# Optimization experiments

Measured on AMD Instinct MI355X. Metric: run time of the kernel, lower is better.

Reference implementation:

```python
import jax, jax.numpy as jnp
import numpy as np

CHEB_K = 3  # from init_kwargs

def _layernorm(v, g, b, eps=1e-12):
    mu = jnp.mean(v, axis=-1, keepdims=True)
    var = jnp.var(v, axis=-1, keepdims=True)  # biased, matches torch LayerNorm
    return (v - mu) * jax.lax.rsqrt(var + eps) * g + b

def setup_inputs() -> dict:
    key = jax.random.key(0)
    ks = jax.random.split(key, 5)
    B, N, D_IN, D_OUT, E = 64, 2048, 64, 64, 16
    return {
        "x": jax.random.normal(ks[0], (B, N, D_IN), dtype=jnp.float32),
        "node_embeddings": jax.random.normal(ks[1], (N, E), dtype=jnp.float32),
        "time_embeddings": jax.random.normal(ks[2], (E,), dtype=jnp.float32),
        "weights_pool": jax.random.normal(ks[3], (E, CHEB_K, D_IN, D_OUT), dtype=jnp.float32) * 0.1,
        "bias_pool": jax.random.normal(ks[4], (E, D_OUT), dtype=jnp.float32) * 0.1,
        "ln_gamma": jnp.ones((E,), dtype=jnp.float32),
        "ln_beta": jnp.zeros((E,), dtype=jnp.float32),
    }

def reference(x, node_embeddings, time_embeddings, weights_pool, bias_pool, ln_gamma, ln_beta):
    N = node_embeddings.shape[0]
    # dropout in eval mode -> identity
    ne = _layernorm(node_embeddings + time_embeddings[None, :], ln_gamma, ln_beta)  # [N,E]
    supports0 = jax.nn.softmax(ne @ ne.T, axis=1)  # [N,N]
    support_set = [jnp.eye(N, dtype=x.dtype), supports0]
    for _ in range(2, CHEB_K):
        support_set.append(2.0 * supports0 @ support_set[-1] - support_set[-2])
    supports = jnp.stack(support_set, axis=0)  # [K,N,N]
    weights = jnp.einsum('nd,dkio->nkio', ne, weights_pool)  # [N,K,I,O]
    bias = ne @ bias_pool  # [N,O]
    x_g = jnp.einsum('knm,bmc->bnkc', supports, x)  # [B,N,K,I]
    return jnp.einsum('bnki,nkio->bno', x_g, weights) + bias  # [B,N,O]
```

## Files before the change

### kernel.cpp

```cpp
#include <hip/hip_runtime.h>
#include <stdint.h>

typedef unsigned short u16;
typedef __attribute__((ext_vector_type(8))) short   bf16x8;
typedef __attribute__((ext_vector_type(4))) float   f32x4;
typedef __attribute__((ext_vector_type(4))) u16     u16x4;
typedef __attribute__((ext_vector_type(8))) u16     u16x8;

#define NN 2048
#define BB 64
#define DD 64
#define XSTRIDE (NN*DD)

__device__ __forceinline__ float bf2f(u16 u) {
    union { unsigned int i; float f; } v; v.i = ((unsigned int)u) << 16; return v.f;
}
__device__ __forceinline__ u16 f2bf(float f) {
    union { float f; unsigned int i; } v; v.f = f;
    unsigned int u = v.i;
    return (u16)((u + 0x7fffu + ((u >> 16) & 1u)) >> 16);
}

typedef __attribute__((address_space(3))) unsigned int lds_u32_t;
typedef const __attribute__((address_space(1))) unsigned int g_u32_t;
__device__ __forceinline__ void gload_lds16(const void* g, void* l) {
    __builtin_amdgcn_global_load_lds((g_u32_t*)(uintptr_t)g, (lds_u32_t*)(uintptr_t)l, 16, 0, 0);
}

__global__ __launch_bounds__(256) void k_ln(const float* __restrict__ nodee,
                                            const float* __restrict__ timee,
                                            const float* __restrict__ gamma,
                                            const float* __restrict__ beta,
                                            float* __restrict__ ne,
                                            u16* __restrict__ neb) {
    int n = blockIdx.x * 256 + threadIdx.x;
    float v[16]; float mu = 0.f;
    const float4* p = (const float4*)(nodee + (long)n * 16);
#pragma unroll
    for (int i = 0; i < 4; i++) {
        float4 q = p[i];
        v[i*4+0]=q.x; v[i*4+1]=q.y; v[i*4+2]=q.z; v[i*4+3]=q.w;
    }
#pragma unroll
    for (int e = 0; e < 16; e++) { v[e] += timee[e]; mu += v[e]; }
    mu *= (1.f/16.f);
    float var = 0.f;
#pragma unroll
    for (int e = 0; e < 16; e++) { float d = v[e]-mu; var += d*d; }
    var *= (1.f/16.f);
    float rs = rsqrtf(var + 1e-12f);
    float4* o = (float4*)(ne + (long)n * 16);
    u16x8 nb[2];
#pragma unroll
    for (int i = 0; i < 4; i++) {
        float4 q;
        q.x = (v[i*4+0]-mu)*rs*gamma[i*4+0] + beta[i*4+0];
        q.y = (v[i*4+1]-mu)*rs*gamma[i*4+1] + beta[i*4+1];
        q.z = (v[i*4+2]-mu)*rs*gamma[i*4+2] + beta[i*4+2];
        q.w = (v[i*4+3]-mu)*rs*gamma[i*4+3] + beta[i*4+3];
        o[i] = q;
        nb[i>>1][(i&1)*4+0] = f2bf(q.x); nb[i>>1][(i&1)*4+1] = f2bf(q.y);
        nb[i>>1][(i&1)*4+2] = f2bf(q.z); nb[i>>1][(i&1)*4+3] = f2bf(q.w);
    }
    u16x8 z;
#pragma unroll
    for (int j = 0; j < 8; j++) z[j] = 0;
    u16x8* ob = (u16x8*)&neb[(long)n * 32];
    ob[0] = nb[0]; ob[1] = nb[1]; ob[2] = z; ob[3] = z;
}

__global__ __launch_bounds__(256) void k_wperm(const float* __restrict__ wp,
                                               u16* __restrict__ wpP) {
    int j = blockIdx.x * 256 + threadIdx.x;
    int o = j / 192, ki = j - o * 192;
    int src = ki * 64 + o;
    u16x8 ov[4];
#pragma unroll
    for (int e = 0; e < 16; e++) ov[e>>3][e&7] = f2bf(wp[(long)e*12288 + src]);
#pragma unroll
    for (int e = 0; e < 8; e++) { ov[2][e] = 0; ov[3][e] = 0; }
    u16x8* dst = (u16x8*)&wpP[(long)j * 32];
    dst[0]=ov[0]; dst[1]=ov[1]; dst[2]=ov[2]; dst[3]=ov[3];
}

__global__ __launch_bounds__(256) void k_softmax(const float* __restrict__ ne,
                                                 u16* __restrict__ S) {
    __shared__ float row[2048];
    __shared__ float red[8];
    int n = blockIdx.x, t = threadIdx.x;
    int wave = t >> 6, lane = t & 63;
    f32x4 nev[4];
#pragma unroll
    for (int i = 0; i < 4; i++) nev[i] = *(const f32x4*)&ne[n*16 + i*4];
    float lmax = -1e30f;
    for (int m = t; m < 2048; m += 256) {
        const f32x4* p = (const f32x4*)&ne[m*16];
        f32x4 d4 = nev[0]*p[0] + nev[1]*p[1] + nev[2]*p[2] + nev[3]*p[3];
        float d = d4[0]+d4[1]+d4[2]+d4[3];
        row[m] = d;
        lmax = fmaxf(lmax, d);
    }
#pragma unroll
    for (int off = 32; off > 0; off >>= 1) lmax = fmaxf(lmax, __shfl_xor(lmax, off));
    if (lane == 0) red[wave] = lmax;
    __syncthreads();
    float gmax = fmaxf(fmaxf(red[0], red[1]), fmaxf(red[2], red[3]));
    float lsum = 0.f;
    for (int m = t; m < 2048; m += 256) {
        float ev = __expf(row[m] - gmax);
        row[m] = ev;
        lsum += ev;
    }
#pragma unroll
    for (int off = 32; off > 0; off >>= 1) lsum += __shfl_xor(lsum, off);
    __syncthreads();
    if (lane == 0) red[wave] = lsum;
    __syncthreads();
    float inv = 1.f / (red[0]+red[1]+red[2]+red[3]);
    for (int m = t; m < 2048; m += 256)
        S[(long)n*2048 + m] = f2bf(row[m] * inv);
}

__global__ __launch_bounds__(256) void k_permute(const float* __restrict__ x,
                                                 u16* __restrict__ Xpt) {
    __shared__ u16 T[64][72];
    int bid = blockIdx.x;
    int b = bid >> 5, m0 = (bid & 31) * 64;
    int t = threadIdx.x;
#pragma unroll
    for (int it = 0; it < 4; it++) {
        int fi = it*256 + t;
        int row = fi >> 4, c4 = (fi & 15) * 4;
        float4 v = *(const float4*)&x[(long)b*XSTRIDE + (m0+row)*64 + c4];
        T[c4+0][row] = f2bf(v.x); T[c4+1][row] = f2bf(v.y);
        T[c4+2][row] = f2bf(v.z); T[c4+3][row] = f2bf(v.w);
    }
    __syncthreads();
#pragma unroll
    for (int it = 0; it < 2; it++) {
        int ch = it*256 + t;
        int c = ch >> 3, m8 = (ch & 7) * 8;
        u16x8 v = *(const u16x8*)&T[c][m8];
        *(u16x8*)&Xpt[(long)(b*64 + c)*2048 + m0 + m8] = v;
    }
}

__global__ __launch_bounds__(256) void k_gemm_bt(const u16* __restrict__ A,
                                                 const u16* __restrict__ Bt,
                                                 u16* __restrict__ C,
                                                 int M, int Ncols, int K) {
    __shared__ __align__(16) u16 As[128*32];
    __shared__ __align__(16) u16 Bs[128*32];
    const int t = threadIdx.x;
    const int wave = t >> 6, lane = t & 63;
    const int l15 = lane & 15, lhi = lane >> 4;
    const int m0 = blockIdx.y * 128;
    const int n0 = blockIdx.x * 128;
    const int wr = wave >> 1, wc = wave & 1;
    f32x4 acc[4][4] = {};
    const int srow = t >> 2;
    const int sk = (t & 3) * 8;
    const u16* gA = A + (long)(m0 + srow) * K + sk;
    const u16* gB = Bt + (long)(n0 + srow) * K + sk;
    const long half = (long)64 * K;
    u16* lA = As + wave * 512;
    u16* lB = Bs + wave * 512;
    const int aoff = (wr*64 + l15)*32 + lhi*8;
    const int boff = (wc*64 + l15)*32 + lhi*8;
    for (int k0 = 0; k0 < K; k0 += 32) {
        gload_lds16(gA + k0,        lA);
        gload_lds16(gA + k0 + half, lA + 2048);
        gload_lds16(gB + k0,        lB);
        gload_lds16(gB + k0 + half, lB + 2048);
        __syncthreads();
        bf16x8 af[4], bv[4];
#pragma unroll
        for (int m = 0; m < 4; m++) af[m] = *(const bf16x8*)&As[aoff + m*512];
#pragma unroll
        for (int q = 0; q < 4; q++) bv[q] = *(const bf16x8*)&Bs[boff + q*512];
#pragma unroll
        for (int m = 0; m < 4; m++)
#pragma unroll
            for (int q = 0; q < 4; q++)
                acc[m][q] = __builtin_amdgcn_mfma_f32_16x16x32_bf16(af[m], bv[q], acc[m][q], 0, 0, 0);
        __syncthreads();
    }
#pragma unroll
    for (int m = 0; m < 4; m++) {
        int row = m0 + wr*64 + m*16 + lhi*4;
#pragma unroll
        for (int q = 0; q < 4; q++) {
            int col = n0 + wc*64 + q*16 + l15;
#pragma unroll
            for (int r = 0; r < 4; r++)
                C[(long)(row + r) * Ncols + col] = f2bf(acc[m][q][r]);
        }
    }
}

__global__ __launch_bounds__(512, 1) void k_gemm_big(const u16* __restrict__ A,
                                                     const u16* __restrict__ Bt,
                                                     u16* __restrict__ C,
                                                     u16* __restrict__ Ct,
                                                     int M, int Ncols, int K) {
    __shared__ __align__(16) u16 LB[73728];
    const int t = threadIdx.x;
    const int wave = t >> 6, lane = t & 63;
    const int l15 = lane & 15, lhi = lane >> 4;
    const int nwg = gridDim.x * gridDim.y;
    const int wgid = blockIdx.y * gridDim.x + blockIdx.x;
    const int swz = (wgid & 7) * (nwg >> 3) + (wgid >> 3);
    const int by = swz / gridDim.x, bx = swz - by * gridDim.x;
    const int m0 = by * 128, n0 = bx * 256;
    const int wr = wave >> 2, wc = wave & 3;
    const int NT = K >> 6;
    f32x4 acc[4][4] = {};

    const int srow = t >> 3;
    const int sswz = ((t & 7) ^ (srow & 7)) * 8;
    const u16* gA0 = A  + (long)(m0 + srow) * K + sswz;
    const u16* gB0 = Bt + (long)(n0 + srow) * K + sswz;
    const long rP = (long)64 * K;
    const int ldsW = wave * 512;

    int curA = 0,     nxtA = 8192,  tgtA = 16384;
    int curB = 24576, nxtB = 40960, tgtB = 57344;

    gload_lds16(gA0,           &LB[curA + 0*4096 + ldsW]);
    gload_lds16(gA0 + rP,      &LB[curA + 1*4096 + ldsW]);
#pragma unroll
    for (int r = 0; r < 4; r++) gload_lds16(gB0 + r*rP,      &LB[curB + r*4096 + ldsW]);
    gload_lds16(gA0 + 64,      &LB[nxtA + 0*4096 + ldsW]);
    gload_lds16(gA0 + rP + 64, &LB[nxtA + 1*4096 + ldsW]);
#pragma unroll
    for (int r = 0; r < 4; r++) gload_lds16(gB0 + r*rP + 64, &LB[nxtB + r*4096 + ldsW]);
    asm volatile("s_waitcnt vmcnt(6)" ::: "memory");
    __builtin_amdgcn_s_barrier();
    asm volatile("" ::: "memory");

    const int rsw = l15 & 7;
    const int sw0 = (lhi ^ rsw) * 8;
    const int sw1 = ((4 + lhi) ^ rsw) * 8;
    const int abase = (wr*64 + l15) * 64;
    const int bbase = (wc*64 + l15) * 64;

#pragma unroll 1
    for (int tt = 0; tt < NT; tt++) {
        const bool stg = (tt + 2 < NT);
        const long ko2 = (long)((tt + 2) << 6);
        {
            bf16x8 af[4], bv[4];
#pragma unroll
            for (int m = 0; m < 4; m++) af[m] = *(const bf16x8*)&LB[curA + abase + m*1024 + sw0];
#pragma unroll
            for (int q = 0; q < 4; q++) bv[q] = *(const bf16x8*)&LB[curB + bbase + q*1024 + sw0];
            if (stg) {
                gload_lds16(gA0 + ko2,      &LB[tgtA + 0*4096 + ldsW]);
                gload_lds16(gA0 + rP + ko2, &LB[tgtA + 1*4096 + ldsW]);
                gload_lds16(gB0 + ko2,      &LB[tgtB + 0*4096 + ldsW]);
            }
            __builtin_amdgcn_s_setprio(1);
#pragma unroll
            for (int m = 0; m < 4; m++)
#pragma unroll
                for (int q = 0; q < 4; q++)
                    acc[m][q] = __builtin_amdgcn_mfma_f32_16x16x32_bf16(af[m], bv[q], acc[m][q], 0, 0, 0);
            __builtin_amdgcn_s_setprio(0);
        }
        {
            bf16x8 af[4], bv[4];
#pragma unroll
            for (int m = 0; m < 4; m++) af[m] = *(const bf16x8*)&LB[curA + abase + m*1024 + sw1];
#pragma unroll
            for (int q = 0; q < 4; q++) bv[q] = *(const bf16x8*)&LB[curB + bbase + q*1024 + sw1];
            if (stg) {
                gload_lds16(gB0 + 1*rP + ko2, &LB[tgtB + 1*4096 + ldsW]);
                gload_lds16(gB0 + 2*rP + ko2, &LB[tgtB + 2*4096 + ldsW]);
                gload_lds16(gB0 + 3*rP + ko2, &LB[tgtB + 3*4096 + ldsW]);
            }
            __builtin_amdgcn_s_setprio(1);
#pragma unroll
            for (int m = 0; m < 4; m++)
#pragma unroll
                for (int q = 0; q < 4; q++)
                    acc[m][q] = __builtin_amdgcn_mfma_f32_16x16x32_bf16(af[m], bv[q], acc[m][q], 0, 0, 0);
            __builtin_amdgcn_s_setprio(0);
        }
        asm volatile("" ::: "memory");
        if (stg)                asm volatile("s_waitcnt vmcnt(6)" ::: "memory");
        else if (tt + 1 < NT)   asm volatile("s_waitcnt vmcnt(0)" ::: "memory");
        if (tt + 1 < NT) {
            __builtin_amdgcn_s_barrier();
            asm volatile("" ::: "memory");
        }
        int ta = curA; curA = nxtA; nxtA = tgtA; tgtA = ta;
        int tb = curB; curB = nxtB; nxtB = tgtB; tgtB = tb;
    }
#pragma unroll
    for (int m = 0; m < 4; m++) {
        int row = m0 + wr*64 + m*16 + lhi*4;
#pragma unroll
        for (int q = 0; q < 4; q++) {
            int col = n0 + wc*64 + q*16 + l15;
#pragma unroll
            for (int r = 0; r < 4; r++)
                C[(long)(row + r) * Ncols + col] = f2bf(acc[m][q][r]);
        }
    }
    if (Ct != nullptr) {
        __syncthreads();
#pragma unroll
        for (int m = 0; m < 4; m++) {
            int rowb = wr*64 + m*16 + lhi*4;
#pragma unroll
            for (int q = 0; q < 4; q++) {
                int col = wc*64 + q*16 + l15;
                u16x4 p;
                p[0]=f2bf(acc[m][q][0]); p[1]=f2bf(acc[m][q][1]);
                p[2]=f2bf(acc[m][q][2]); p[3]=f2bf(acc[m][q][3]);
                *(u16x4*)&LB[col*136 + rowb] = p;
            }
        }
        __syncthreads();
        const int j16 = t >> 4, ch = (t & 15) * 8;
#pragma unroll
        for (int p = 0; p < 8; p++) {
            int j = p*32 + j16;
            u16x8 v = *(const u16x8*)&LB[j*136 + ch];
            *(u16x8*)&Ct[(long)(n0 + j)*M + m0 + ch] = v;
        }
    }
}

__global__ __launch_bounds__(256) void k_final(const float* __restrict__ x,
                                               const u16* __restrict__ Y1,
                                               const u16* __restrict__ Y2,
                                               const u16* __restrict__ Wt,
                                               const float* __restrict__ ne,
                                               const float* __restrict__ bp,
                                               float* __restrict__ out) {
    __shared__ __align__(16) u16 Al[64*200];
    __shared__ __align__(16) u16 Wl[64*200];
    __shared__ float biasl[64];
    int n = blockIdx.x;
    int t = threadIdx.x;
    int wave = t >> 6, lane = t & 63;
    int l15 = lane & 15, lhi = lane >> 4;
#pragma unroll
    for (int it = 0; it < 6; it++) {
        int ch = it*256 + t;
        int o = ch / 24, kl = (ch % 24) * 8;
        u16x8 v = *(const u16x8*)&Wt[(long)n*12288 + ch*8];
        *(u16x8*)&Wl[o*200 + kl] = v;
    }
    float xs[16];
#pragma unroll
    for (int it = 0; it < 4; it++) {
        int fi = it*256 + t;
        int b = fi >> 4, i4 = (fi & 15) * 4;
        float4 v = *(const float4*)&x[(long)b*XSTRIDE + n*64 + i4];
        xs[it*4+0]=v.x; xs[it*4+1]=v.y; xs[it*4+2]=v.z; xs[it*4+3]=v.w;
        u16x4 p; p[0]=f2bf(v.x); p[1]=f2bf(v.y); p[2]=f2bf(v.z); p[3]=f2bf(v.w);
        *(u16x4*)&Al[b*200 + i4] = p;
    }
#pragma unroll
    for (int it = 0; it < 2; it++) {
        int ch = it*256 + t;
        int b = ch >> 3, i8 = (ch & 7)*8;
        u16x8 v = *(const u16x8*)&Y1[(long)n*4096 + ch*8];
        *(u16x8*)&Al[b*200 + 64 + i8] = v;
    }
#pragma unroll
    for (int it = 0; it < 4; it++) {
        int fi = it*256 + t;
        int b = fi >> 4, i4 = (fi & 15)*4;
        u16x4 y = *(const u16x4*)&Y2[(long)n*4096 + fi*4];
        u16x4 p;
#pragma unroll
        for (int j = 0; j < 4; j++) p[j] = f2bf(2.f*bf2f(y[j]) - xs[it*4+j]);
        *(u16x4*)&Al[b*200 + 128 + i4] = p;
    }
    if (t < 64) {
        float s = 0.f;
#pragma unroll
        for (int e = 0; e < 16; e++) s += ne[n*16+e] * bp[e*64 + t];
        biasl[t] = s;
    }
    __syncthreads();
    f32x4 acc[4] = {};
#pragma unroll
    for (int kk = 0; kk < 6; kk++) {
        bf16x8 bv = *(const bf16x8*)&Wl[(wave*16 + l15)*200 + kk*32 + lhi*8];
#pragma unroll
        for (int m = 0; m < 4; m++) {
            bf16x8 av = *(const bf16x8*)&Al[(m*16 + l15)*200 + kk*32 + lhi*8];
            acc[m] = __builtin_amdgcn_mfma_f32_16x16x32_bf16(av, bv, acc[m], 0, 0, 0);
        }
    }
    int o = wave*16 + l15;
    float bias = biasl[o];
#pragma unroll
    for (int m = 0; m < 4; m++) {
        int brow = m*16 + lhi*4;
#pragma unroll
        for (int r = 0; r < 4; r++)
            out[(long)(brow + r)*XSTRIDE + n*64 + o] = acc[m][r] + bias;
    }
}

extern "C" void kernel_launch(void* const* d_in, const int* in_sizes, int n_in,
                              void* d_out, int out_size, void* d_ws, size_t ws_size,
                              hipStream_t stream) {
    const float* x     = (const float*)d_in[0];
    const float* nodee = (const float*)d_in[1];
    const float* timee = (const float*)d_in[2];
    const float* wp    = (const float*)d_in[3];
    const float* bp    = (const float*)d_in[4];
    const float* gamma = (const float*)d_in[5];
    const float* beta  = (const float*)d_in[6];
    float* out = (float*)d_out;

    char* ws = (char*)d_ws;
    float* ne  = (float*)(ws);
    u16* S     = (u16*)(ws + 131072);
    u16* Xpt   = (u16*)(ws + 8519680);
    u16* Y1    = (u16*)(ws + 25296896);
    u16* Y1t   = (u16*)(ws + 42074112);
    u16* Y2    = (u16*)(ws + 58851328);
    u16* Wt    = (u16*)(ws + 75628544);
    u16* neb   = (u16*)(ws + 58851328);
    u16* wpP   = (u16*)(ws + 58851328 + 131072);
    if (ws_size < (size_t)125960192) return;

    k_ln      <<<8,    256, 0, stream>>>(nodee, timee, gamma, beta, ne, neb);
    k_wperm   <<<48,   256, 0, stream>>>(wp, wpP);
    k_gemm_bt <<<dim3(96,16), 256, 0, stream>>>(neb, wpP, Wt, 2048, 12288, 32);
    k_softmax <<<2048, 256, 0, stream>>>(ne, S);
    k_permute <<<2048, 256, 0, stream>>>(x, Xpt);
    k_gemm_big<<<dim3(16,16), 512, 0, stream>>>(S, Xpt, Y1, Y1t, 2048, 4096, 2048);
    k_gemm_big<<<dim3(16,16), 512, 0, stream>>>(S, Y1t, Y2, (u16*)nullptr, 2048, 4096, 2048);
    k_final   <<<2048, 256, 0, stream>>>(x, Y1, Y2, Wt, ne, bp, out);
}
```

Before: 150.7 us.

## Split K across wave pairs in big GEMM with LDS reduction

```diff
diff --git a/kernel.cpp b/kernel.cpp
--- a/kernel.cpp
+++ b/kernel.cpp
@@ -198,7 +198,7 @@
     }
 }
 
-__global__ __launch_bounds__(512, 1) void k_gemm_big(const u16* __restrict__ A,
+__global__ __launch_bounds__(512, 2) void k_gemm_big(const u16* __restrict__ A,
                                                      const u16* __restrict__ Bt,
                                                      u16* __restrict__ C,
                                                      u16* __restrict__ Ct,
@@ -212,9 +212,11 @@
     const int swz = (wgid & 7) * (nwg >> 3) + (wgid >> 3);
     const int by = swz / gridDim.x, bx = swz - by * gridDim.x;
     const int m0 = by * 128, n0 = bx * 256;
-    const int wr = wave >> 2, wc = wave & 3;
+    const int kwv = wave & 1;
+    const int ws  = wave >> 1;
+    const int wr = ws >> 1, wc = ws & 1;
     const int NT = K >> 6;
-    f32x4 acc[4][4] = {};
+    f32x4 acc[4][8] = {};
 
     const int srow = t >> 3;
     const int sswz = ((t & 7) ^ (srow & 7)) * 8;
@@ -239,53 +241,34 @@
     asm volatile("" ::: "memory");
 
     const int rsw = l15 & 7;
-    const int sw0 = (lhi ^ rsw) * 8;
-    const int sw1 = ((4 + lhi) ^ rsw) * 8;
-    const int abase = (wr*64 + l15) * 64;
-    const int bbase = (wc*64 + l15) * 64;
+    const int swk = ((kwv*4 + lhi) ^ rsw) * 8;
+    const int abase = (wr*64  + l15) * 64;
+    const int bbase = (wc*128 + l15) * 64;
 
 #pragma unroll 1
     for (int tt = 0; tt < NT; tt++) {
         const bool stg = (tt + 2 < NT);
         const long ko2 = (long)((tt + 2) << 6);
-        {
-            bf16x8 af[4], bv[4];
-#pragma unroll
-            for (int m = 0; m < 4; m++) af[m] = *(const bf16x8*)&LB[curA + abase + m*1024 + sw0];
-#pragma unroll
-            for (int q = 0; q < 4; q++) bv[q] = *(const bf16x8*)&LB[curB + bbase + q*1024 + sw0];
-            if (stg) {
-                gload_lds16(gA0 + ko2,      &LB[tgtA + 0*4096 + ldsW]);
-                gload_lds16(gA0 + rP + ko2, &LB[tgtA + 1*4096 + ldsW]);
-                gload_lds16(gB0 + ko2,      &LB[tgtB + 0*4096 + ldsW]);
-            }
-            __builtin_amdgcn_s_setprio(1);
-#pragma unroll
-            for (int m = 0; m < 4; m++)
-#pragma unroll
-                for (int q = 0; q < 4; q++)
-                    acc[m][q] = __builtin_amdgcn_mfma_f32_16x16x32_bf16(af[m], bv[q], acc[m][q], 0, 0, 0);
-            __builtin_amdgcn_s_setprio(0);
-        }
-        {
-            bf16x8 af[4], bv[4];
-#pragma unroll
-            for (int m = 0; m < 4; m++) af[m] = *(const bf16x8*)&LB[curA + abase + m*1024 + sw1];
-#pragma unroll
-            for (int q = 0; q < 4; q++) bv[q] = *(const bf16x8*)&LB[curB + bbase + q*1024 + sw1];
-            if (stg) {
-                gload_lds16(gB0 + 1*rP + ko2, &LB[tgtB + 1*4096 + ldsW]);
-                gload_lds16(gB0 + 2*rP + ko2, &LB[tgtB + 2*4096 + ldsW]);
-                gload_lds16(gB0 + 3*rP + ko2, &LB[tgtB + 3*4096 + ldsW]);
-            }
-            __builtin_amdgcn_s_setprio(1);
-#pragma unroll
-            for (int m = 0; m < 4; m++)
-#pragma unroll
-                for (int q = 0; q < 4; q++)
-                    acc[m][q] = __builtin_amdgcn_mfma_f32_16x16x32_bf16(af[m], bv[q], acc[m][q], 0, 0, 0);
-            __builtin_amdgcn_s_setprio(0);
-        }
+        bf16x8 af[4], bv[8];
+#pragma unroll
+        for (int m = 0; m < 4; m++) af[m] = *(const bf16x8*)&LB[curA + abase + m*1024 + swk];
+#pragma unroll
+        for (int q = 0; q < 8; q++) bv[q] = *(const bf16x8*)&LB[curB + bbase + q*1024 + swk];
+        if (stg) {
+            gload_lds16(gA0 + ko2,        &LB[tgtA + 0*4096 + ldsW]);
+            gload_lds16(gA0 + rP + ko2,   &LB[tgtA + 1*4096 + ldsW]);
+            gload_lds16(gB0 + ko2,        &LB[tgtB + 0*4096 + ldsW]);
+            gload_lds16(gB0 + 1*rP + ko2, &LB[tgtB + 1*4096 + ldsW]);
+            gload_lds16(gB0 + 2*rP + ko2, &LB[tgtB + 2*4096 + ldsW]);
+            gload_lds16(gB0 + 3*rP + ko2, &LB[tgtB + 3*4096 + ldsW]);
+        }
+        __builtin_amdgcn_s_setprio(1);
+#pragma unroll
+        for (int m = 0; m < 4; m++)
+#pragma unroll
+            for (int q = 0; q < 8; q++)
+                acc[m][q] = __builtin_amdgcn_mfma_f32_16x16x32_bf16(af[m], bv[q], acc[m][q], 0, 0, 0);
+        __builtin_amdgcn_s_setprio(0);
         asm volatile("" ::: "memory");
         if (stg)                asm volatile("s_waitcnt vmcnt(6)" ::: "memory");
         else if (tt + 1 < NT)   asm volatile("s_waitcnt vmcnt(0)" ::: "memory");
@@ -296,38 +279,61 @@
         int ta = curA; curA = nxtA; nxtA = tgtA; tgtA = ta;
         int tb = curB; curB = nxtB; nxtB = tgtB; tgtB = tb;
     }
-#pragma unroll
-    for (int m = 0; m < 4; m++) {
-        int row = m0 + wr*64 + m*16 + lhi*4;
-#pragma unroll
-        for (int q = 0; q < 4; q++) {
-            int col = n0 + wc*64 + q*16 + l15;
-#pragma unroll
-            for (int r = 0; r < 4; r++)
-                C[(long)(row + r) * Ncols + col] = f2bf(acc[m][q][r]);
+
+    float* LBf = (float*)LB;
+    __syncthreads();
+    if (kwv == 1) {
+        const int base = ws*8192 + lane*4;
+#pragma unroll
+        for (int m = 0; m < 4; m++)
+#pragma unroll
+            for (int q = 0; q < 8; q++)
+                *(f32x4*)&LBf[base + (m*8 + q)*256] = acc[m][q];
+    }
+    __syncthreads();
+    if (kwv == 0) {
+        const int base = ws*8192 + lane*4;
+#pragma unroll
+        for (int m = 0; m < 4; m++)
+#pragma unroll
+            for (int q = 0; q < 8; q++) {
+                f32x4 p = *(const f32x4*)&LBf[base + (m*8 + q)*256];
+                acc[m][q] += p;
+            }
+#pragma unroll
+        for (int m = 0; m < 4; m++) {
+            int row = m0 + wr*64 + m*16 + lhi*4;
+#pragma unroll
+            for (int q = 0; q < 8; q++) {
+                int col = n0 + wc*128 + q*16 + l15;
+#pragma unroll
+                for (int r = 0; r < 4; r++)
+                    C[(long)(row + r) * Ncols + col] = f2bf(acc[m][q][r]);
+            }
         }
     }
     if (Ct != nullptr) {
         __syncthreads();
-#pragma unroll
-        for (int m = 0; m < 4; m++) {
-            int rowb = wr*64 + m*16 + lhi*4;
-#pragma unroll
-            for (int q = 0; q < 4; q++) {
-                int col = wc*64 + q*16 + l15;
-                u16x4 p;
-                p[0]=f2bf(acc[m][q][0]); p[1]=f2bf(acc[m][q][1]);
-                p[2]=f2bf(acc[m][q][2]); p[3]=f2bf(acc[m][q][3]);
-                *(u16x4*)&LB[col*136 + rowb] = p;
+        if (kwv == 0) {
+#pragma unroll
+            for (int m = 0; m < 4; m++) {
+                int rowb = wr*64 + m*16 + lhi*4;
+#pragma unroll
+                for (int q = 0; q < 8; q++) {
+                    int col = wc*128 + q*16 + l15;
+                    u16x4 p;
+                    p[0]=f2bf(acc[m][q][0]); p[1]=f2bf(acc[m][q][1]);
+                    p[2]=f2bf(acc[m][q][2]); p[3]=f2bf(acc[m][q][3]);
+                    *(u16x4*)&LB[col*144 + rowb] = p;
+                }
             }
         }
         __syncthreads();
-        const int j16 = t >> 4, ch = (t & 15) * 8;
+        const int j = t >> 1, ch0 = (t & 1) * 64;
 #pragma unroll
         for (int p = 0; p < 8; p++) {
-            int j = p*32 + j16;
-            u16x8 v = *(const u16x8*)&LB[j*136 + ch];
-            *(u16x8*)&Ct[(long)(n0 + j)*M + m0 + ch] = v;
+            u16x8 v = *(const u16x8*)&LB[j*144 + ch0 + p*8];
+            *(u16x8*)&Ct[(long)(n0 + j)*M + m0 + ch0 + p*8] = v;
         }
     }
 }
```

New measurement: 157.2 us. 1.04x slower.

## Batch softmax rows, emit node-major bf16 x copy, reorder weight GEMM

Applied to the files above, without the earlier changes.

```diff
diff --git a/kernel.cpp b/kernel.cpp
--- a/kernel.cpp
+++ b/kernel.cpp
@@ -85,44 +85,72 @@
 
 __global__ __launch_bounds__(256) void k_softmax(const float* __restrict__ ne,
                                                  u16* __restrict__ S) {
-    __shared__ float row[2048];
-    __shared__ float red[8];
-    int n = blockIdx.x, t = threadIdx.x;
+    __shared__ float row[4][2048];
+    __shared__ float red[4][4];
+    int n0 = blockIdx.x * 4, t = threadIdx.x;
     int wave = t >> 6, lane = t & 63;
-    f32x4 nev[4];
-#pragma unroll
-    for (int i = 0; i < 4; i++) nev[i] = *(const f32x4*)&ne[n*16 + i*4];
-    float lmax = -1e30f;
+    f32x4 nev[4][4];
+#pragma unroll
+    for (int r = 0; r < 4; r++)
+#pragma unroll
+        for (int i = 0; i < 4; i++) nev[r][i] = *(const f32x4*)&ne[(n0+r)*16 + i*4];
+    float lmax[4] = {-1e30f, -1e30f, -1e30f, -1e30f};
     for (int m = t; m < 2048; m += 256) {
         const f32x4* p = (const f32x4*)&ne[m*16];
-        f32x4 d4 = nev[0]*p[0] + nev[1]*p[1] + nev[2]*p[2] + nev[3]*p[3];
-        float d = d4[0]+d4[1]+d4[2]+d4[3];
-        row[m] = d;
-        lmax = fmaxf(lmax, d);
-    }
-#pragma unroll
-    for (int off = 32; off > 0; off >>= 1) lmax = fmaxf(lmax, __shfl_xor(lmax, off));
-    if (lane == 0) red[wave] = lmax;
+        f32x4 p0 = p[0], p1 = p[1], p2 = p[2], p3 = p[3];
+#pragma unroll
+        for (int r = 0; r < 4; r++) {
+            f32x4 d4 = nev[r][0]*p0 + nev[r][1]*p1 + nev[r][2]*p2 + nev[r][3]*p3;
+            float d = d4[0]+d4[1]+d4[2]+d4[3];
+            row[r][m] = d;
+            lmax[r] = fmaxf(lmax[r], d);
+        }
+    }
+#pragma unroll
+    for (int r = 0; r < 4; r++)
+#pragma unroll
+        for (int off = 32; off > 0; off >>= 1) lmax[r] = fmaxf(lmax[r], __shfl_xor(lmax[r], off));
+    if (lane == 0) {
+#pragma unroll
+        for (int r = 0; r < 4; r++) red[r][wave] = lmax[r];
+    }
     __syncthreads();
-    float gmax = fmaxf(fmaxf(red[0], red[1]), fmaxf(red[2], red[3]));
-    float lsum = 0.f;
+    float gmax[4], lsum[4] = {0.f, 0.f, 0.f, 0.f};
+#pragma unroll
+    for (int r = 0; r < 4; r++)
+        gmax[r] = fmaxf(fmaxf(red[r][0], red[r][1]), fmaxf(red[r][2], red[r][3]));
     for (int m = t; m < 2048; m += 256) {
-        float ev = __expf(row[m] - gmax);
-        row[m] = ev;
-        lsum += ev;
-    }
-#pragma unroll
-    for (int off = 32; off > 0; off >>= 1) lsum += __shfl_xor(lsum, off);
+#pragma unroll
+        for (int r = 0; r < 4; r++) {
+            float ev = __expf(row[r][m] - gmax[r]);
+            row[r][m] = ev;
+            lsum[r] += ev;
+        }
+    }
+#pragma unroll
+    for (int r = 0; r < 4; r++)
+#pragma unroll
+        for (int off = 32; off > 0; off >>= 1) lsum[r] += __shfl_xor(lsum[r], off);
     __syncthreads();
-    if (lane == 0) red[wave] = lsum;
+    if (lane == 0) {
+#pragma unroll
+        for (int r = 0; r < 4; r++) red[r][wave] = lsum[r];
+    }
     __syncthreads();
-    float inv = 1.f / (red[0]+red[1]+red[2]+red[3]);
-    for (int m = t; m < 2048; m += 256)
-        S[(long)n*2048 + m] = f2bf(row[m] * inv);
+    float inv[4];
+#pragma unroll
+    for (int r = 0; r < 4; r++)
+        inv[r] = 1.f / (red[r][0] + red[r][1] + red[r][2] + red[r][3]);
+    for (int m = t; m < 2048; m += 256) {
+#pragma unroll
+        for (int r = 0; r < 4; r++)
+            S[(long)(n0+r)*2048 + m] = f2bf(row[r][m] * inv[r]);
+    }
 }
 
 __global__ __launch_bounds__(256) void k_permute(const float* __restrict__ x,
-                                                 u16* __restrict__ Xpt) {
+                                                 u16* __restrict__ Xpt,
+                                                 u16* __restrict__ Xb) {
     __shared__ u16 T[64][72];
     int bid = blockIdx.x;
     int b = bid >> 5, m0 = (bid & 31) * 64;
@@ -142,6 +170,14 @@
         int c = ch >> 3, m8 = (ch & 7) * 8;
         u16x8 v = *(const u16x8*)&T[c][m8];
         *(u16x8*)&Xpt[(long)(b*64 + c)*2048 + m0 + m8] = v;
+    }
+#pragma unroll
+    for (int it = 0; it < 4; it++) {
+        int wi = it*256 + t;
+        int m = wi >> 4, c4 = (wi & 15) * 4;
+        u16x4 v;
+        v[0] = T[c4+0][m]; v[1] = T[c4+1][m]; v[2] = T[c4+2][m]; v[3] = T[c4+3][m];
+        *(u16x4*)&Xb[(long)(m0 + m)*4096 + b*64 + c4] = v;
     }
 }
 
@@ -332,7 +368,7 @@
     }
 }
 
-__global__ __launch_bounds__(256) void k_final(const float* __restrict__ x,
+__global__ __launch_bounds__(256) void k_final(const u16* __restrict__ Xb,
                                                const u16* __restrict__ Y1,
                                                const u16* __restrict__ Y2,
                                                const u16* __restrict__ Wt,
@@ -353,15 +389,17 @@
         u16x8 v = *(const u16x8*)&Wt[(long)n*12288 + ch*8];
         *(u16x8*)&Wl[o*200 + kl] = v;
     }
-    float xs[16];
-#pragma unroll
-    for (int it = 0; it < 4; it++) {
-        int fi = it*256 + t;
-        int b = fi >> 4, i4 = (fi & 15) * 4;
-        float4 v = *(const float4*)&x[(long)b*XSTRIDE + n*64 + i4];
-        xs[it*4+0]=v.x; xs[it*4+1]=v.y; xs[it*4+2]=v.z; xs[it*4+3]=v.w;
-        u16x4 p; p[0]=f2bf(v.x); p[1]=f2bf(v.y); p[2]=f2bf(v.z); p[3]=f2bf(v.w);
-        *(u16x4*)&Al[b*200 + i4] = p;
+#pragma unroll
+    for (int it = 0; it < 2; it++) {
+        int ch = it*256 + t;
+        int b = ch >> 3, i8 = (ch & 7) * 8;
+        u16x8 xv = *(const u16x8*)&Xb[(long)n*4096 + ch*8];
+        *(u16x8*)&Al[b*200 + i8] = xv;
+        u16x8 yv = *(const u16x8*)&Y2[(long)n*4096 + ch*8];
+        u16x8 p;
+#pragma unroll
+        for (int j = 0; j < 8; j++) p[j] = f2bf(2.f*bf2f(yv[j]) - bf2f(xv[j]));
+        *(u16x8*)&Al[b*200 + 128 + i8] = p;
     }
 #pragma unroll
     for (int it = 0; it < 2; it++) {
@@ -369,16 +407,6 @@
         int b = ch >> 3, i8 = (ch & 7)*8;
         u16x8 v = *(const u16x8*)&Y1[(long)n*4096 + ch*8];
         *(u16x8*)&Al[b*200 + 64 + i8] = v;
-    }
-#pragma unroll
-    for (int it = 0; it < 4; it++) {
-        int fi = it*256 + t;
-        int b = fi >> 4, i4 = (fi & 15)*4;
-        u16x4 y = *(const u16x4*)&Y2[(long)n*4096 + fi*4];
-        u16x4 p;
-#pragma unroll
-        for (int j = 0; j < 4; j++) p[j] = f2bf(2.f*bf2f(y[j]) - xs[it*4+j]);
-        *(u16x4*)&Al[b*200 + 128 + i4] = p;
     }
     if (t < 64) {
         float s = 0.f;
@@ -428,16 +456,17 @@
     u16* Y1t   = (u16*)(ws + 42074112);
     u16* Y2    = (u16*)(ws + 58851328);
     u16* Wt    = (u16*)(ws + 75628544);
-    u16* neb   = (u16*)(ws + 58851328);
-    u16* wpP   = (u16*)(ws + 58851328 + 131072);
-    if (ws_size < (size_t)125960192) return;
+    u16* neb   = (u16*)(ws + 125960192);
+    u16* wpP   = (u16*)(ws + 126091264);
+    u16* Xb    = (u16*)(ws + 127664128);
+    if (ws_size < (size_t)144441344) return;
 
     k_ln      <<<8,    256, 0, stream>>>(nodee, timee, gamma, beta, ne, neb);
     k_wperm   <<<48,   256, 0, stream>>>(wp, wpP);
-    k_gemm_bt <<<dim3(96,16), 256, 0, stream>>>(neb, wpP, Wt, 2048, 12288, 32);
-    k_softmax <<<2048, 256, 0, stream>>>(ne, S);
-    k_permute <<<2048, 256, 0, stream>>>(x, Xpt);
+    k_softmax <<<512,  256, 0, stream>>>(ne, S);
+    k_permute <<<2048, 256, 0, stream>>>(x, Xpt, Xb);
     k_gemm_big<<<dim3(16,16), 512, 0, stream>>>(S, Xpt, Y1, Y1t, 2048, 4096, 2048);
     k_gemm_big<<<dim3(16,16), 512, 0, stream>>>(S, Y1t, Y2, (u16*)nullptr, 2048, 4096, 2048);
-    k_final   <<<2048, 256, 0, stream>>>(x, Y1, Y2, Wt, ne, bp, out);
-}
+    k_gemm_bt <<<dim3(96,16), 256, 0, stream>>>(neb, wpP, Wt, 2048, 12288, 32);
+    k_final   <<<2048, 256, 0, stream>>>(Xb, Y1, Y2, Wt, ne, bp, out);
+}
```

Result: faster. 140.6 us (-6.7%).
